# Performance work log

Measured on AMD Instinct MI355X. Metric: run time of the kernel, lower is better.

## Reference

```python
import jax, jax.numpy as jnp
import numpy as np
import math

DIM = 1024
NUM_HEADS = 16
HEAD_DIM = DIM // NUM_HEADS
EPS = 1e-6
DILATED = 2
WINDOW = 2  # window_size init arg; actual window = L * WINDOW per side


def setup_inputs() -> dict:
    key = jax.random.key(0)
    ks = jax.random.split(key, 14)
    B, S = 1, 8704
    x = jax.random.normal(ks[0], (B, S, DIM), jnp.float32)
    ang = jax.random.uniform(ks[1], (S, HEAD_DIM // 2), jnp.float32, -jnp.pi, jnp.pi)
    freqs_cos = jnp.cos(ang)
    freqs_sin = jnp.sin(ang)
    def lin(k):
        return 0.02 * jax.random.normal(k, (DIM, DIM), jnp.float32)
    def bias(k):
        return 0.01 * jax.random.normal(k, (DIM,), jnp.float32)
    return {
        'x': x, 'freqs_cos': freqs_cos, 'freqs_sin': freqs_sin,
        'wq': lin(ks[2]), 'bq': bias(ks[3]),
        'wk': lin(ks[4]), 'bk': bias(ks[5]),
        'wv': lin(ks[6]), 'bv': bias(ks[7]),
        'wo': lin(ks[8]), 'bo': bias(ks[9]),
        'gq': 1.0 + 0.02 * jax.random.normal(ks[10], (DIM,), jnp.float32),
        'gk': 1.0 + 0.02 * jax.random.normal(ks[11], (DIM,), jnp.float32),
        'f': 34, 'L': 256,
    }


def rmsnorm(h, g):
    return h * jax.lax.rsqrt(jnp.mean(h * h, axis=-1, keepdims=True) + EPS) * g


def rope(h, cos, sin):
    # h: [B,S,D] viewed as interleaved complex pairs per head, rotated by unit freqs
    B, S, D = h.shape
    hp = h.reshape(B, S, NUM_HEADS, HEAD_DIM // 2, 2)
    a, b = hp[..., 0], hp[..., 1]
    c = cos[None, :, None, :]
    s = sin[None, :, None, :]
    ra = a * c - b * s
    rb = a * s + b * c
    return jnp.stack([ra, rb], axis=-1).reshape(B, S, D)


def windowed_attention(q, k, v, w):
    # sliding-window attention: query i attends keys j with |i-j| <= w (inclusive)
    B, S, D = q.shape
    H, hd = NUM_HEADS, HEAD_DIM
    def heads(t):
        return t.reshape(B, S, H, hd).transpose(0, 2, 1, 3)  # [B,H,S,hd]
    qh, kh, vh = heads(q), heads(k), heads(v)
    C = w  # block size == window -> only 3 neighbor key blocks per query block
    pad = (-S) % C
    Sp = S + pad
    nb = Sp // C
    def blocks(t):
        return jnp.pad(t, ((0, 0), (0, 0), (0, pad), (0, 0))).reshape(B, H, nb, C, hd)
    qb = blocks(qh)
    def win(t):
        tb = jnp.pad(blocks(t), ((0, 0), (0, 0), (1, 1), (0, 0), (0, 0)))
        return jnp.concatenate([tb[:, :, i:i + nb] for i in range(3)], axis=3)  # [B,H,nb,3C,hd]
    kw_, vw_ = win(kh), win(vh)
    scores = jnp.einsum('bhnqd,bhnkd->bhnqk', qb, kw_) * (1.0 / math.sqrt(hd))
    qi = jnp.arange(nb)[:, None, None] * C + jnp.arange(C)[None, :, None]      # [nb,C,1]
    kj = (jnp.arange(nb)[:, None, None] - 1) * C + jnp.arange(3 * C)[None, None, :]  # [nb,1,3C]
    valid = (kj >= 0) & (kj < S) & (qi - kj <= w) & (kj - qi <= w)
    scores = jnp.where(valid, scores, -1e9)
    p = jax.nn.softmax(scores, axis=-1)
    o = jnp.einsum('bhnqk,bhnkd->bhnqd', p, vw_)
    return o.reshape(B, H, Sp, hd)[:, :, :S].transpose(0, 2, 1, 3).reshape(B, S, D)


def reference(x, freqs_cos, freqs_sin, wq, bq, wk, bk, wv, bv, wo, bo, gq, gk, f, L):
    B, S, D = x.shape
    q = rope(rmsnorm(x @ wq + bq, gq), freqs_cos, freqs_sin)
    k = rope(rmsnorm(x @ wk + bk, gk), freqs_cos, freqs_sin)
    v = x @ wv + bv
    w = L * WINDOW
    use_dilated = DILATED > 1 and S // (DILATED * L) > 1
    if use_dilated:
        blk = DILATED * L
        pad_len = blk - S % blk  # == blk when S % blk == 0 (faithful to torch code)
        Sp = S + pad_len
        n = Sp // blk
        def padd(t):
            return jnp.pad(t, ((0, 0), (0, pad_len), (0, 0)))
        def dil(t):
            # 'b (n d l) c -> (b d) (n l) c'
            return t.reshape(B, n, DILATED, L, D).transpose(0, 2, 1, 3, 4).reshape(B * DILATED, n * L, D)
        q, k, v = dil(padd(q)), dil(padd(k)), dil(padd(v))
    o = windowed_attention(q, k, v, w)
    out = o @ wo + bo
    if use_dilated:
        # '(b d) (n l) c -> b (n d l) c', then drop pad
        out = out.reshape(B, DILATED, n, L, D).transpose(0, 2, 1, 3, 4).reshape(B, n * DILATED * L, D)
        out = out[:, :S]
    return out
```

## Files before the change

kernel.cpp:

```cpp
#include <hip/hip_runtime.h>
#include <hip/hip_bf16.h>
#include <stdint.h>

#define DIM 1024
#define NH 16
#define HD 64
#define S_ORIG 8704
#define WIN 512

typedef __attribute__((ext_vector_type(8))) short short8;
typedef __attribute__((ext_vector_type(4))) float f32x4;

__device__ __forceinline__ float bf2f(unsigned short u) {
    return __uint_as_float(((unsigned int)u) << 16);
}
__device__ __forceinline__ unsigned short f2bf(float f) {
    unsigned int x = __float_as_uint(f);
    unsigned int r = x + 0x7fffu + ((x >> 16) & 1u);
    return (unsigned short)(r >> 16);
}
__device__ __forceinline__ unsigned int cvtpk(float lo, float hi) {
    unsigned int r;
    asm("v_cvt_pk_bf16_f32 %0, %1, %2" : "=v"(r) : "v"(lo), "v"(hi));
    return r;
}
__device__ __forceinline__ float fexp2(float x) {
#if __has_builtin(__builtin_amdgcn_exp2f)
    return __builtin_amdgcn_exp2f(x);
#else
    float r;
    asm("v_exp_f32 %0, %1" : "=v"(r) : "v"(x));
    return r;
#endif
}

#define GLD_LDS(gptr, lptr) \
    __builtin_amdgcn_global_load_lds((const __attribute__((address_space(1))) void*)(gptr), \
                                     (__attribute__((address_space(3))) void*)(lptr), 16, 0, 0)

#define FBAR() do { __asm__ volatile("" ::: "memory"); \
                    __builtin_amdgcn_s_barrier(); \
                    __asm__ volatile("" ::: "memory"); } while (0)

__global__ __launch_bounds__(256) void prep(const float* __restrict__ x,
                                            unsigned short* __restrict__ xb,
                                            const float* __restrict__ w0,
                                            const float* __restrict__ w1,
                                            const float* __restrict__ w2,
                                            const float* __restrict__ w3,
                                            unsigned short* __restrict__ wt) {
    __shared__ float ts[64][65];
    const int bx = blockIdx.x;
    const int t = threadIdx.x;
    if (bx < 8704) {
        int i = (bx * 256 + t) * 4;
        float4 v = *(const float4*)(x + i);
        ushort4 o;
        o.x = f2bf(v.x); o.y = f2bf(v.y); o.z = f2bf(v.z); o.w = f2bf(v.w);
        *(ushort4*)(xb + i) = o;
        return;
    }
    const int b = bx - 8704;
    const int z = b >> 8;
    const int rem = b & 255;
    const int kb = (rem >> 4) * 64, nb = (rem & 15) * 64;
    const float* w = z == 0 ? w0 : z == 1 ? w1 : z == 2 ? w2 : w3;
    unsigned short* o = wt + (size_t)z * DIM * DIM;
    const int c = t & 63, r4 = t >> 6;
#pragma unroll
    for (int rr = 0; rr < 16; rr++) {
        int row = rr * 4 + r4;
        ts[row][c] = w[(size_t)(kb + row) * DIM + nb + c];
    }
    __syncthreads();
#pragma unroll
    for (int rr = 0; rr < 16; rr++) {
        int nl = rr * 4 + r4;
        o[(size_t)(nb + nl) * DIM + kb + c] = f2bf(ts[c][nl]);
    }
}

__device__ __forceinline__ void gemm_step(const unsigned short* __restrict__ pa,
                                          const unsigned short* __restrict__ pb,
                                          int wr, int wc, int r, int jsw,
                                          f32x4 acc[4][4]) {
    short8 af[4], bfr[4];
#pragma unroll
    for (int i = 0; i < 4; i++)
        af[i] = *(const short8*)&pa[(wr * 64 + i * 16 + r) * 32 + jsw];
#pragma unroll
    for (int j = 0; j < 4; j++)
        bfr[j] = *(const short8*)&pb[(wc * 64 + j * 16 + r) * 32 + jsw];
#pragma unroll
    for (int i = 0; i < 4; i++)
#pragma unroll
        for (int j = 0; j < 4; j++)
            acc[i][j] = __builtin_amdgcn_mfma_f32_16x16x32_bf16(af[i], bfr[j], acc[i][j], 0, 0, 0);
}

template <int OUTF32>
__global__ __launch_bounds__(256) void gemm_bf16(const unsigned short* __restrict__ A,
                                                 const unsigned short* __restrict__ Bt,
                                                 const float* __restrict__ b0,
                                                 const float* __restrict__ b1,
                                                 const float* __restrict__ b2,
                                                 void* __restrict__ Cout) {
    __shared__ __align__(16) unsigned short As[3][128 * 32];
    __shared__ __align__(16) unsigned short Bs[3][128 * 32];
    const int z = blockIdx.z;
    const unsigned short* B = Bt + (size_t)z * DIM * DIM;
    const float* bias = z == 0 ? b0 : (z == 1 ? b1 : b2);
    const int m0 = blockIdx.x * 128, n0 = blockIdx.y * 128;
    const int tid = threadIdx.x;
    const int lane = tid & 63, wv = tid >> 6;
    const int wr = wv >> 1, wc = wv & 1;
    const int quad = lane >> 4, r = lane & 15;

    f32x4 acc[4][4];
#pragma unroll
    for (int i = 0; i < 4; i++)
#pragma unroll
        for (int j = 0; j < 4; j++)
#pragma unroll
            for (int t4 = 0; t4 < 4; t4++) acc[i][j][t4] = 0.0f;

    const unsigned short* a_base = A + (size_t)m0 * DIM;
    const unsigned short* b_base = B + (size_t)n0 * DIM;
    const int c0 = wv * 128 + lane;
    const int r0 = c0 >> 2, o0 = (((c0 & 3) ^ ((c0 >> 3) & 3))) * 8;
    const int c1 = c0 + 64;
    const int r1 = c1 >> 2, o1 = (((c1 & 3) ^ ((c1 >> 3) & 3))) * 8;
    const int ld0 = (wv * 128) * 8, ld1 = (wv * 128 + 64) * 8;

    const int jsw = (quad ^ ((r >> 1) & 3)) * 8;

#define ISSUE_STEP(k0_, abuf_, bbuf_) do {                                  \
        GLD_LDS(a_base + (size_t)r0 * DIM + (k0_) + o0, (abuf_) + ld0);     \
        GLD_LDS(a_base + (size_t)r1 * DIM + (k0_) + o1, (abuf_) + ld1);     \
        GLD_LDS(b_base + (size_t)r0 * DIM + (k0_) + o0, (bbuf_) + ld0);     \
        GLD_LDS(b_base + (size_t)r1 * DIM + (k0_) + o1, (bbuf_) + ld1);     \
    } while (0)

    unsigned short *pa0 = &As[0][0], *pa1 = &As[1][0], *pa2 = &As[2][0];
    unsigned short *pb0 = &Bs[0][0], *pb1 = &Bs[1][0], *pb2 = &Bs[2][0];

    ISSUE_STEP(0, pa0, pb0);
    ISSUE_STEP(32, pa1, pb1);

#pragma unroll 3
    for (int k0 = 0; k0 < DIM - 64; k0 += 32) {
        FBAR();
        ISSUE_STEP(k0 + 64, pa2, pb2);
        __asm__ volatile("s_waitcnt vmcnt(8)" ::: "memory");
        __builtin_amdgcn_sched_barrier(0);
        FBAR();
        gemm_step(pa0, pb0, wr, wc, r, jsw, acc);
        unsigned short* t;
        t = pa0; pa0 = pa1; pa1 = pa2; pa2 = t;
        t = pb0; pb0 = pb1; pb1 = pb2; pb2 = t;
    }
    __asm__ volatile("s_waitcnt vmcnt(4)" ::: "memory");
    __builtin_amdgcn_sched_barrier(0);
    FBAR();
    gemm_step(pa0, pb0, wr, wc, r, jsw, acc);
    {
        unsigned short* t;
        t = pa0; pa0 = pa1; pa1 = pa2; pa2 = t;
        t = pb0; pb0 = pb1; pb1 = pb2; pb2 = t;
    }
    __asm__ volatile("s_waitcnt vmcnt(0)" ::: "memory");
    __builtin_amdgcn_sched_barrier(0);
    FBAR();
    gemm_step(pa0, pb0, wr, wc, r, jsw, acc);
#undef ISSUE_STEP

#pragma unroll
    for (int i = 0; i < 4; i++) {
        const int row = m0 + wr * 64 + i * 16 + quad * 4;
#pragma unroll
        for (int j = 0; j < 4; j++) {
            const int col = n0 + wc * 64 + j * 16 + r;
            const float bvl = bias[col];
#pragma unroll
            for (int t4 = 0; t4 < 4; t4++) {
                float vv = acc[i][j][t4] + bvl;
                if (OUTF32) {
                    ((float*)Cout)[(size_t)(row + t4) * DIM + col] = vv;
                } else {
                    ((unsigned short*)Cout)[(size_t)z * S_ORIG * DIM + (size_t)(row + t4) * DIM + col] = f2bf(vv);
                }
            }
        }
    }
}

__global__ __launch_bounds__(256) void norm_rope(unsigned short* __restrict__ hq,
                                                 unsigned short* __restrict__ hk,
                                                 const float* __restrict__ gq,
                                                 const float* __restrict__ gk,
                                                 const float* __restrict__ fcos,
                                                 const float* __restrict__ fsin) {
    const int z = blockIdx.y;
    unsigned short* h = z == 0 ? hq : hk;
    const float* g = z == 0 ? gq : gk;
    const int w = threadIdx.x >> 6, lane = threadIdx.x & 63;
    const int srow = blockIdx.x * 4 + w;
    unsigned short* hp = h + (size_t)srow * DIM;
    const int p0 = lane * 8, p1 = 512 + lane * 8;

    union { int4 i4; unsigned short u[8]; } r0, r1, o0, o1;
    r0.i4 = *(const int4*)(hp + p0);
    r1.i4 = *(const int4*)(hp + p1);
    float v[16];
#pragma unroll
    for (int j = 0; j < 8; j++) { v[j] = bf2f(r0.u[j]); v[8 + j] = bf2f(r1.u[j]); }

    float ss = 0.0f;
#pragma unroll
    for (int j = 0; j < 16; j++) ss += v[j] * v[j];
#pragma unroll
    for (int off = 1; off < 64; off <<= 1) ss += __shfl_xor(ss, off, 64);
    const float rinv = rsqrtf(ss * (1.0f / DIM) + 1e-6f);

    float4 ga = *(const float4*)(g + p0), gb = *(const float4*)(g + p0 + 4);
    float4 gc = *(const float4*)(g + p1), gd = *(const float4*)(g + p1 + 4);
    const float* gg[4] = {&ga.x, &gb.x, &gc.x, &gd.x};
#pragma unroll
    for (int q4 = 0; q4 < 4; q4++)
#pragma unroll
        for (int j = 0; j < 4; j++) v[q4 * 4 + j] *= rinv * gg[q4][j];

    const int i0 = (p0 & 63) >> 1;
    float4 cs = *(const float4*)(fcos + (size_t)srow * 32 + i0);
    float4 sn = *(const float4*)(fsin + (size_t)srow * 32 + i0);
    const float* cp = &cs.x;
    const float* sp = &sn.x;
#pragma unroll
    for (int seg = 0; seg < 2; seg++) {
        unsigned short* uo = seg == 0 ? o0.u : o1.u;
#pragma unroll
        for (int pr = 0; pr < 4; pr++) {
            const float a = v[seg * 8 + pr * 2], b = v[seg * 8 + pr * 2 + 1];
            uo[pr * 2]     = f2bf(a * cp[pr] - b * sp[pr]);
            uo[pr * 2 + 1] = f2bf(a * sp[pr] + b * cp[pr]);
        }
    }
    *(int4*)(hp + p0) = o0.i4;
    *(int4*)(hp + p1) = o1.i4;
}

__device__ __forceinline__ void qstep(const unsigned short* __restrict__ Ks,
                                      const unsigned short* __restrict__ Vt,
                                      unsigned short* __restrict__ pw,
                                      int jsw0, int jsw1, int quad, int r16,
                                      int kbase, int qi, bool edge,
                                      const short8* __restrict__ qf,
                                      f32x4* __restrict__ oacc, float& lsum) {
    f32x4 sv[4];
#pragma unroll
    for (int nt = 0; nt < 4; nt++) {
        const int row = (nt * 16 + r16) * 64;
        short8 k0f = *(const short8*)&Ks[row + jsw0];
        short8 k1f = *(const short8*)&Ks[row + jsw1];
        f32x4 a = {0.0f, 0.0f, 0.0f, 0.0f};
        a = __builtin_amdgcn_mfma_f32_16x16x32_bf16(k0f, qf[0], a, 0, 0, 0);
        a = __builtin_amdgcn_mfma_f32_16x16x32_bf16(k1f, qf[1], a, 0, 0, 0);
        sv[nt] = a;
    }
#pragma unroll
    for (int nt = 0; nt < 4; nt++) {
        float p[4];
#pragma unroll
        for (int rr = 0; rr < 4; rr++) {
            float e = fexp2(sv[nt][rr]);
            if (edge) {
                const int kj = kbase + nt * 16 + quad * 4 + rr;
                const int dl = qi - kj;
                if (dl > WIN || dl < -WIN) e = 0.0f;
            }
            p[rr] = e;
        }
        lsum += (p[0] + p[1]) + (p[2] + p[3]);
        uint2 pk;
        pk.x = cvtpk(p[0], p[1]);
        pk.y = cvtpk(p[2], p[3]);
        *(uint2*)&pw[r16 * 72 + nt * 16 + quad * 4] = pk;
    }
    __asm__ volatile("s_waitcnt lgkmcnt(0)" ::: "memory");
    short8 pf0 = *(const short8*)&pw[r16 * 72 + quad * 8];
    short8 pf1 = *(const short8*)&pw[r16 * 72 + 32 + quad * 8];
#pragma unroll
    for (int nt = 0; nt < 4; nt++) {
        short8 v0f = *(const short8*)&Vt[(nt * 16 + r16) * 72 + quad * 8];
        short8 v1f = *(const short8*)&Vt[(nt * 16 + r16) * 72 + 32 + quad * 8];
        oacc[nt] = __builtin_amdgcn_mfma_f32_16x16x32_bf16(v0f, pf0, oacc[nt], 0, 0, 0);
        oacc[nt] = __builtin_amdgcn_mfma_f32_16x16x32_bf16(v1f, pf1, oacc[nt], 0, 0, 0);
    }
}

__device__ __forceinline__ void pack_write_v(unsigned short* __restrict__ Vt,
                                             int4 a0i, int4 a1i, int vt_d0, int vt_kk) {
    union { int4 i4; unsigned int w[4]; } a0, a1;
    a0.i4 = a0i; a1.i4 = a1i;
#pragma unroll
    for (int dw = 0; dw < 4; dw++) {
        unsigned int lo = __builtin_amdgcn_perm(a1.w[dw], a0.w[dw], 0x05040100u);
        unsigned int hi = __builtin_amdgcn_perm(a1.w[dw], a0.w[dw], 0x07060302u);
        *(unsigned int*)&Vt[(vt_d0 + dw * 2) * 72 + vt_kk] = lo;
        *(unsigned int*)&Vt[(vt_d0 + dw * 2 + 1) * 72 + vt_kk] = hi;
    }
}

__global__ __launch_bounds__(256) void attn(const unsigned short* __restrict__ qkv,
                                            unsigned short* __restrict__ ob) {
    __shared__ __align__(16) unsigned short Ks[2][64 * 64];
    __shared__ __align__(16) unsigned short Vt[64 * 72];
    __shared__ __align__(16) unsigned short Ps[4][16 * 72];

    const int head = blockIdx.x >> 1;
    const int d = blockIdx.x & 1;
    const int t0 = blockIdx.y * 2, t1 = t0 + 1;
    const int tid = threadIdx.x;
    const int lane = tid & 63, wv = tid >> 6;
    const int quad = lane >> 4, r16 = lane & 15;

    const unsigned short* qb = qkv;
    const unsigned short* kb = qkv + (size_t)S_ORIG * DIM;
    const unsigned short* vb = qkv + (size_t)2 * S_ORIG * DIM;

    const int qi0 = t0 * 64 + wv * 16 + r16;
    const int qi1 = qi0 + 64;
    const int og_q0 = ((qi0 >> 8) << 9) + d * 256 + (qi0 & 255);
    const int og_q1 = ((qi1 >> 8) << 9) + d * 256 + (qi1 & 255);
    short8 qf0[2], qf1[2];
    {
        const float QSC = 0.125f * 1.44269504088896f;
        const unsigned short* qr0 = qb + (size_t)og_q0 * DIM + head * HD + quad * 8;
        const unsigned short* qr1 = qb + (size_t)og_q1 * DIM + head * HD + quad * 8;
#pragma unroll
        for (int c = 0; c < 2; c++) {
            union { int4 i4; unsigned short u[8]; short8 s8; } i0v, i1v, a0v, a1v;
            i0v.i4 = *(const int4*)(qr0 + c * 32);
            i1v.i4 = *(const int4*)(qr1 + c * 32);
#pragma unroll
            for (int j = 0; j < 8; j++) {
                a0v.u[j] = f2bf(bf2f(i0v.u[j]) * QSC);
                a1v.u[j] = f2bf(bf2f(i1v.u[j]) * QSC);
            }
            qf0[c] = a0v.s8;
            qf1[c] = a1v.s8;
        }
    }

    f32x4 oacc0[4], oacc1[4];
    float lsum0 = 0.0f, lsum1 = 0.0f;
#pragma unroll
    for (int nt = 0; nt < 4; nt++)
#pragma unroll
        for (int rr = 0; rr < 4; rr++) { oacc0[nt][rr] = 0.0f; oacc1[nt][rr] = 0.0f; }

    const int kt_lo = (t0 - 8 > 0) ? (t0 - 8) : 0;
    const int kt_hi = (t1 + 8 < 67) ? (t1 + 8) : 67;

    const int krow0 = tid >> 3;
    const int kgc = ((tid & 7) ^ (krow0 & 7)) * 8;

    const int vt_kk = (tid & 31) * 2, vt_d0 = (tid >> 5) * 8;

    const int jsw0 = (quad ^ (r16 & 7)) * 8;
    const int jsw1 = jsw0 ^ 32;

    unsigned short* pw = &Ps[wv][0];

#define ISSUE_K(kbase_, bufb_) do {                                              \
        const int kj0_ = (kbase_) + krow0;                                       \
        const int ok0_ = ((kj0_ >> 8) << 9) + d * 256 + (kj0_ & 255);            \
        GLD_LDS(kb + (size_t)ok0_ * DIM + head * HD + kgc, (bufb_) + wv * 512);  \
        const int kj1_ = kj0_ + 32;                                              \
        const int ok1_ = ((kj1_ >> 8) << 9) + d * 256 + (kj1_ & 255);            \
        GLD_LDS(kb + (size_t)ok1_ * DIM + head * HD + kgc, (bufb_) + 2048 + wv * 512); \
    } while (0)

#define LOAD_V(kbase_, a0_, a1_) do {                                            \
        const int kj_ = (kbase_) + vt_kk;                                        \
        const int ok_ = ((kj_ >> 8) << 9) + d * 256 + (kj_ & 255);               \
        (a0_) = *(const int4*)(vb + (size_t)ok_ * DIM + head * HD + vt_d0);      \
        (a1_) = *(const int4*)(vb + (size_t)(ok_ + 1) * DIM + head * HD + vt_d0);\
    } while (0)

    ISSUE_K(kt_lo * 64, &Ks[0][0]);
    int4 vc0, vc1;
    LOAD_V(kt_lo * 64, vc0, vc1);

    int cur = 0;
    for (int kt = kt_lo; kt <= kt_hi; kt++) {
        const int kbase = kt * 64;
        FBAR();

        const int knb = ((kt < kt_hi) ? (kt + 1) : kt_hi) * 64;
        ISSUE_K(knb, &Ks[cur ^ 1][0]);
        int4 vn0, vn1;
        LOAD_V(knb, vn0, vn1);

        __asm__ volatile("s_waitcnt vmcnt(4)" ::: "memory");
        __builtin_amdgcn_sched_barrier(0);

        pack_write_v(&Vt[0], vc0, vc1, vt_d0, vt_kk);
        __asm__ volatile("s_waitcnt lgkmcnt(0)" ::: "memory");
        FBAR();

        if (kt <= t0 + 8)
            qstep(&Ks[cur][0], Vt, pw, jsw0, jsw1, quad, r16, kbase, qi0,
                  (kt == t0 - 8) || (kt == t0 + 8), qf0, oacc0, lsum0);
        if (kt >= t1 - 8)
            qstep(&Ks[cur][0], Vt, pw, jsw0, jsw1, quad, r16, kbase, qi1,
                  (kt == t1 - 8) || (kt == t1 + 8), qf1, oacc1, lsum1);

        vc0 = vn0; vc1 = vn1;
        cur ^= 1;
    }
#undef ISSUE_K
#undef LOAD_V

    __asm__ volatile("" :: "v"(vc0.x), "v"(vc0.y), "v"(vc0.z), "v"(vc0.w),
                          "v"(vc1.x), "v"(vc1.y), "v"(vc1.z), "v"(vc1.w));
    __asm__ volatile("s_waitcnt vmcnt(0)" ::: "memory");

    lsum0 += __shfl_xor(lsum0, 16, 64);
    lsum0 += __shfl_xor(lsum0, 32, 64);
    lsum1 += __shfl_xor(lsum1, 16, 64);
    lsum1 += __shfl_xor(lsum1, 32, 64);
    {
        const int cnt0 = (qi0 + WIN < 4607 ? qi0 + WIN : 4607) - 4351;
        if (cnt0 > 0) lsum0 += (float)cnt0;
        const int cnt1 = (qi1 + WIN < 4607 ? qi1 + WIN : 4607) - 4351;
        if (cnt1 > 0) lsum1 += (float)cnt1;
    }
    const float linv0 = 1.0f / lsum0;
    const float linv1 = 1.0f / lsum1;

#pragma unroll
    for (int nt = 0; nt < 4; nt++) {
        ushort4 o0, o1;
        o0.x = f2bf(oacc0[nt][0] * linv0);
        o0.y = f2bf(oacc0[nt][1] * linv0);
        o0.z = f2bf(oacc0[nt][2] * linv0);
        o0.w = f2bf(oacc0[nt][3] * linv0);
        *(ushort4*)&ob[(size_t)og_q0 * DIM + head * HD + nt * 16 + quad * 4] = o0;
        o1.x = f2bf(oacc1[nt][0] * linv1);
        o1.y = f2bf(oacc1[nt][1] * linv1);
        o1.z = f2bf(oacc1[nt][2] * linv1);
        o1.w = f2bf(oacc1[nt][3] * linv1);
        *(ushort4*)&ob[(size_t)og_q1 * DIM + head * HD + nt * 16 + quad * 4] = o1;
    }
}

extern "C" void kernel_launch(void* const* d_in, const int* in_sizes, int n_in,
                              void* d_out, int out_size, void* d_ws, size_t ws_size,
                              hipStream_t stream) {
    const float* x    = (const float*)d_in[0];
    const float* fcos = (const float*)d_in[1];
    const float* fsin = (const float*)d_in[2];
    const float* wq   = (const float*)d_in[3];
    const float* bq   = (const float*)d_in[4];
    const float* wk   = (const float*)d_in[5];
    const float* bk   = (const float*)d_in[6];
    const float* wv   = (const float*)d_in[7];
    const float* bv   = (const float*)d_in[8];
    const float* wo   = (const float*)d_in[9];
    const float* bo   = (const float*)d_in[10];
    const float* gq   = (const float*)d_in[11];
    const float* gk   = (const float*)d_in[12];

    char* ws = (char*)d_ws;
    unsigned short* xb = (unsigned short*)(ws);
    unsigned short* wt = (unsigned short*)(ws + 17825792);
    unsigned short* h  = (unsigned short*)(ws + 26214400);
    unsigned short* ob = (unsigned short*)(ws + 79691776);
    float* outp = (float*)d_out;

    prep<<<9728, 256, 0, stream>>>(x, xb, wq, wk, wv, wo, wt);
    gemm_bf16<0><<<dim3(68, 8, 3), 256, 0, stream>>>(xb, wt, bq, bk, bv, (void*)h);
    norm_rope<<<dim3(2176, 2), 256, 0, stream>>>(h, h + (size_t)S_ORIG * DIM, gq, gk, fcos, fsin);
    attn<<<dim3(32, 34), 256, 0, stream>>>(h, ob);
    gemm_bf16<1><<<dim3(68, 8, 1), 256, 0, stream>>>(ob, wt + (size_t)3 * DIM * DIM, bo, bo, bo, (void*)outp);
}
```

Before: 302.6 us.

## Switch attention to 32x32x16 MFMA with register-resident P via permlane32 swap

New measurement: 305.4 us. Within noise of the previous version (+0.9%).

```diff
diff --git a/kernel.cpp b/kernel.cpp
--- a/kernel.cpp
+++ b/kernel.cpp
@@ -10,6 +10,7 @@
 
 typedef __attribute__((ext_vector_type(8))) short short8;
 typedef __attribute__((ext_vector_type(4))) float f32x4;
+typedef __attribute__((ext_vector_type(16))) float f32x16;
 
 __device__ __forceinline__ float bf2f(unsigned short u) {
     return __uint_as_float(((unsigned int)u) << 16);
@@ -249,115 +250,85 @@
     *(int4*)(hp + p1) = o1.i4;
 }
 
-__device__ __forceinline__ void qstep(const unsigned short* __restrict__ Ks,
-                                      const unsigned short* __restrict__ Vt,
-                                      unsigned short* __restrict__ pw,
-                                      int jsw0, int jsw1, int quad, int r16,
-                                      int kbase, int qi, bool edge,
-                                      const short8* __restrict__ qf,
-                                      f32x4* __restrict__ oacc, float& lsum) {
-    f32x4 sv[4];
-#pragma unroll
-    for (int nt = 0; nt < 4; nt++) {
-        const int row = (nt * 16 + r16) * 64;
-        short8 k0f = *(const short8*)&Ks[row + jsw0];
-        short8 k1f = *(const short8*)&Ks[row + jsw1];
-        f32x4 a = {0.0f, 0.0f, 0.0f, 0.0f};
-        a = __builtin_amdgcn_mfma_f32_16x16x32_bf16(k0f, qf[0], a, 0, 0, 0);
-        a = __builtin_amdgcn_mfma_f32_16x16x32_bf16(k1f, qf[1], a, 0, 0, 0);
-        sv[nt] = a;
-    }
-#pragma unroll
-    for (int nt = 0; nt < 4; nt++) {
-        float p[4];
-#pragma unroll
-        for (int rr = 0; rr < 4; rr++) {
-            float e = fexp2(sv[nt][rr]);
-            if (edge) {
-                const int kj = kbase + nt * 16 + quad * 4 + rr;
-                const int dl = qi - kj;
-                if (dl > WIN || dl < -WIN) e = 0.0f;
-            }
-            p[rr] = e;
+__device__ __forceinline__ void softmax16(f32x16& s, int kk0, int hi4, int qi,
+                                          bool edge, float& lsum) {
+#pragma unroll
+    for (int reg = 0; reg < 16; reg++) {
+        float e = fexp2(s[reg]);
+        if (edge) {
+            const int kj = kk0 + (reg & 3) + 8 * (reg >> 2) + hi4;
+            const int dl = qi - kj;
+            if (dl > WIN || dl < -WIN) e = 0.0f;
         }
-        lsum += (p[0] + p[1]) + (p[2] + p[3]);
-        uint2 pk;
-        pk.x = cvtpk(p[0], p[1]);
-        pk.y = cvtpk(p[2], p[3]);
-        *(uint2*)&pw[r16 * 72 + nt * 16 + quad * 4] = pk;
-    }
-    __asm__ volatile("s_waitcnt lgkmcnt(0)" ::: "memory");
-    short8 pf0 = *(const short8*)&pw[r16 * 72 + quad * 8];
-    short8 pf1 = *(const short8*)&pw[r16 * 72 + 32 + quad * 8];
-#pragma unroll
-    for (int nt = 0; nt < 4; nt++) {
-        short8 v0f = *(const short8*)&Vt[(nt * 16 + r16) * 72 + quad * 8];
-        short8 v1f = *(const short8*)&Vt[(nt * 16 + r16) * 72 + 32 + quad * 8];
-        oacc[nt] = __builtin_amdgcn_mfma_f32_16x16x32_bf16(v0f, pf0, oacc[nt], 0, 0, 0);
-        oacc[nt] = __builtin_amdgcn_mfma_f32_16x16x32_bf16(v1f, pf1, oacc[nt], 0, 0, 0);
-    }
+        s[reg] = e;
+        lsum += e;
+    }
+}
+
+__device__ __forceinline__ short8 mkfrag(const f32x16& p, int base) {
+    unsigned int a0 = cvtpk(p[base + 0], p[base + 1]);
+    unsigned int b0 = cvtpk(p[base + 4], p[base + 5]);
+    unsigned int a1 = cvtpk(p[base + 2], p[base + 3]);
+    unsigned int b1 = cvtpk(p[base + 6], p[base + 7]);
+    asm volatile("v_permlane32_swap_b32 %0, %1" : "+v"(a0), "+v"(b0));
+    asm volatile("v_permlane32_swap_b32 %0, %1" : "+v"(a1), "+v"(b1));
+    union { unsigned int w[4]; short8 s; } u;
+    u.w[0] = a0; u.w[1] = a1; u.w[2] = b0; u.w[3] = b1;
+    return u.s;
 }
 
 __device__ __forceinline__ void pack_write_v(unsigned short* __restrict__ Vt,
-                                             int4 a0i, int4 a1i, int vt_d0, int vt_kk) {
+                                             int4 a0i, int4 a1i, int vt_d0, int vkc, int vko) {
     union { int4 i4; unsigned int w[4]; } a0, a1;
     a0.i4 = a0i; a1.i4 = a1i;
 #pragma unroll
     for (int dw = 0; dw < 4; dw++) {
         unsigned int lo = __builtin_amdgcn_perm(a1.w[dw], a0.w[dw], 0x05040100u);
-        unsigned int hi = __builtin_amdgcn_perm(a1.w[dw], a0.w[dw], 0x07060302u);
-        *(unsigned int*)&Vt[(vt_d0 + dw * 2) * 72 + vt_kk] = lo;
-        *(unsigned int*)&Vt[(vt_d0 + dw * 2 + 1) * 72 + vt_kk] = hi;
+        unsigned int hw = __builtin_amdgcn_perm(a1.w[dw], a0.w[dw], 0x07060302u);
+        *(unsigned int*)&Vt[(vt_d0 + dw * 2) * 64 + ((vkc ^ (dw * 2)) << 3) + vko] = lo;
+        *(unsigned int*)&Vt[(vt_d0 + dw * 2 + 1) * 64 + ((vkc ^ (dw * 2 + 1)) << 3) + vko] = hw;
     }
 }
 
 __global__ __launch_bounds__(256) void attn(const unsigned short* __restrict__ qkv,
                                             unsigned short* __restrict__ ob) {
     __shared__ __align__(16) unsigned short Ks[2][64 * 64];
-    __shared__ __align__(16) unsigned short Vt[64 * 72];
-    __shared__ __align__(16) unsigned short Ps[4][16 * 72];
+    __shared__ __align__(16) unsigned short Vt[64 * 64];
 
     const int head = blockIdx.x >> 1;
     const int d = blockIdx.x & 1;
     const int t0 = blockIdx.y * 2, t1 = t0 + 1;
     const int tid = threadIdx.x;
     const int lane = tid & 63, wv = tid >> 6;
-    const int quad = lane >> 4, r16 = lane & 15;
+    const int hi = lane >> 5, q32 = lane & 31;
+    const int sw8 = (q32 & 7);
 
     const unsigned short* qb = qkv;
     const unsigned short* kb = qkv + (size_t)S_ORIG * DIM;
     const unsigned short* vb = qkv + (size_t)2 * S_ORIG * DIM;
 
-    const int qi0 = t0 * 64 + wv * 16 + r16;
-    const int qi1 = qi0 + 64;
-    const int og_q0 = ((qi0 >> 8) << 9) + d * 256 + (qi0 & 255);
-    const int og_q1 = ((qi1 >> 8) << 9) + d * 256 + (qi1 & 255);
-    short8 qf0[2], qf1[2];
+    const int tw = t0 + (wv >> 1);
+    const int qi = tw * 64 + (wv & 1) * 32 + q32;
+    const int og_q = ((qi >> 8) << 9) + d * 256 + (qi & 255);
+
+    short8 qf[4];
     {
         const float QSC = 0.125f * 1.44269504088896f;
-        const unsigned short* qr0 = qb + (size_t)og_q0 * DIM + head * HD + quad * 8;
-        const unsigned short* qr1 = qb + (size_t)og_q1 * DIM + head * HD + quad * 8;
-#pragma unroll
-        for (int c = 0; c < 2; c++) {
-            union { int4 i4; unsigned short u[8]; short8 s8; } i0v, i1v, a0v, a1v;
-            i0v.i4 = *(const int4*)(qr0 + c * 32);
-            i1v.i4 = *(const int4*)(qr1 + c * 32);
-#pragma unroll
-            for (int j = 0; j < 8; j++) {
-                a0v.u[j] = f2bf(bf2f(i0v.u[j]) * QSC);
-                a1v.u[j] = f2bf(bf2f(i1v.u[j]) * QSC);
-            }
-            qf0[c] = a0v.s8;
-            qf1[c] = a1v.s8;
+        const unsigned short* qrow = qb + (size_t)og_q * DIM + head * HD + hi * 8;
+#pragma unroll
+        for (int kd = 0; kd < 4; kd++) {
+            union { int4 i4; unsigned short u[8]; short8 s8; } iv, ov;
+            iv.i4 = *(const int4*)(qrow + kd * 16);
+#pragma unroll
+            for (int j = 0; j < 8; j++) ov.u[j] = f2bf(bf2f(iv.u[j]) * QSC);
+            qf[kd] = ov.s8;
         }
     }
 
-    f32x4 oacc0[4], oacc1[4];
-    float lsum0 = 0.0f, lsum1 = 0.0f;
-#pragma unroll
-    for (int nt = 0; nt < 4; nt++)
-#pragma unroll
-        for (int rr = 0; rr < 4; rr++) { oacc0[nt][rr] = 0.0f; oacc1[nt][rr] = 0.0f; }
+    f32x16 o0, o1;
+#pragma unroll
+    for (int i = 0; i < 16; i++) { o0[i] = 0.0f; o1[i] = 0.0f; }
+    float lsum = 0.0f;
 
     const int kt_lo = (t0 - 8 > 0) ? (t0 - 8) : 0;
     const int kt_hi = (t1 + 8 < 67) ? (t1 + 8) : 67;
@@ -366,11 +337,7 @@
     const int kgc = ((tid & 7) ^ (krow0 & 7)) * 8;
 
     const int vt_kk = (tid & 31) * 2, vt_d0 = (tid >> 5) * 8;
-
-    const int jsw0 = (quad ^ (r16 & 7)) * 8;
-    const int jsw1 = jsw0 ^ 32;
-
-    unsigned short* pw = &Ps[wv][0];
+    const int vkc = vt_kk >> 3, vko = vt_kk & 7;
 
 #define ISSUE_K(kbase_, bufb_) do {                                              \
         const int kj0_ = (kbase_) + krow0;                                       \
@@ -405,16 +372,42 @@
         __asm__ volatile("s_waitcnt vmcnt(4)" ::: "memory");
         __builtin_amdgcn_sched_barrier(0);
 
-        pack_write_v(&Vt[0], vc0, vc1, vt_d0, vt_kk);
+        pack_write_v(&Vt[0], vc0, vc1, vt_d0, vkc, vko);
         __asm__ volatile("s_waitcnt lgkmcnt(0)" ::: "memory");
         FBAR();
 
-        if (kt <= t0 + 8)
-            qstep(&Ks[cur][0], Vt, pw, jsw0, jsw1, quad, r16, kbase, qi0,
-                  (kt == t0 - 8) || (kt == t0 + 8), qf0, oacc0, lsum0);
-        if (kt >= t1 - 8)
-            qstep(&Ks[cur][0], Vt, pw, jsw0, jsw1, quad, r16, kbase, qi1,
-                  (kt == t1 - 8) || (kt == t1 + 8), qf1, oacc1, lsum1);
+        if (kt >= tw - 8 && kt <= tw + 8) {
+            const bool edge = (kt == tw - 8) || (kt == tw + 8);
+            const unsigned short* K = &Ks[cur][0];
+
+            f32x16 s0, s1;
+#pragma unroll
+            for (int i = 0; i < 16; i++) { s0[i] = 0.0f; s1[i] = 0.0f; }
+#pragma unroll
+            for (int kd = 0; kd < 4; kd++) {
+                const int c = ((kd * 2 + hi) ^ sw8) << 3;
+                short8 k0 = *(const short8*)&K[q32 * 64 + c];
+                short8 k1 = *(const short8*)&K[(32 + q32) * 64 + c];
+                s0 = __builtin_amdgcn_mfma_f32_32x32x16_bf16(k0, qf[kd], s0, 0, 0, 0);
+                s1 = __builtin_amdgcn_mfma_f32_32x32x16_bf16(k1, qf[kd], s1, 0, 0, 0);
+            }
+
+            const int hi4 = hi * 4;
+            softmax16(s0, kbase, hi4, qi, edge, lsum);
+            softmax16(s1, kbase + 32, hi4, qi, edge, lsum);
+            short8 pf0 = mkfrag(s0, 0), pf1 = mkfrag(s0, 8);
+            short8 pf2 = mkfrag(s1, 0), pf3 = mkfrag(s1, 8);
+
+#pragma unroll
+            for (int kw = 0; kw < 4; kw++) {
+                const int c = ((kw * 2 + hi) ^ sw8) << 3;
+                short8 v0 = *(const short8*)&Vt[q32 * 64 + c];
+                short8 v1 = *(const short8*)&Vt[(32 + q32) * 64 + c];
+                const short8 pf = kw == 0 ? pf0 : kw == 1 ? pf1 : kw == 2 ? pf2 : pf3;
+                o0 = __builtin_amdgcn_mfma_f32_32x32x16_bf16(v0, pf, o0, 0, 0, 0);
+                o1 = __builtin_amdgcn_mfma_f32_32x32x16_bf16(v1, pf, o1, 0, 0, 0);
+            }
+        }
 
         vc0 = vn0; vc1 = vn1;
         cur ^= 1;
@@ -426,32 +419,27 @@
                           "v"(vc1.x), "v"(vc1.y), "v"(vc1.z), "v"(vc1.w));
     __asm__ volatile("s_waitcnt vmcnt(0)" ::: "memory");
 
-    lsum0 += __shfl_xor(lsum0, 16, 64);
-    lsum0 += __shfl_xor(lsum0, 32, 64);
-    lsum1 += __shfl_xor(lsum1, 16, 64);
-    lsum1 += __shfl_xor(lsum1, 32, 64);
+    lsum += __shfl_xor(lsum, 32, 64);
     {
-        const int cnt0 = (qi0 + WIN < 4607 ? qi0 + WIN : 4607) - 4351;
-        if (cnt0 > 0) lsum0 += (float)cnt0;
-        const int cnt1 = (qi1 + WIN < 4607 ? qi1 + WIN : 4607) - 4351;
-        if (cnt1 > 0) lsum1 += (float)cnt1;
-    }
-    const float linv0 = 1.0f / lsum0;
-    const float linv1 = 1.0f / lsum1;
-
-#pragma unroll
-    for (int nt = 0; nt < 4; nt++) {
-        ushort4 o0, o1;
-        o0.x = f2bf(oacc0[nt][0] * linv0);
-        o0.y = f2bf(oacc0[nt][1] * linv0);
-        o0.z = f2bf(oacc0[nt][2] * linv0);
-        o0.w = f2bf(oacc0[nt][3] * linv0);
-        *(ushort4*)&ob[(size_t)og_q0 * DIM + head * HD + nt * 16 + quad * 4] = o0;
-        o1.x = f2bf(oacc1[nt][0] * linv1);
-        o1.y = f2bf(oacc1[nt][1] * linv1);
-        o1.z = f2bf(oacc1[nt][2] * linv1);
-        o1.w = f2bf(oacc1[nt][3] * linv1);
-        *(ushort4*)&ob[(size_t)og_q1 * DIM + head * HD + nt * 16 + quad * 4] = o1;
+        const int cnt = (qi + WIN < 4607 ? qi + WIN : 4607) - 4351;
+        if (cnt > 0) lsum += (float)cnt;
+    }
+    const float linv = 1.0f / lsum;
+
+    unsigned short* obase = ob + (size_t)og_q * DIM + head * HD + hi * 4;
+#pragma unroll
+    for (int g = 0; g < 4; g++) {
+        ushort4 u0, u1;
+        u0.x = f2bf(o0[g * 4 + 0] * linv);
+        u0.y = f2bf(o0[g * 4 + 1] * linv);
+        u0.z = f2bf(o0[g * 4 + 2] * linv);
+        u0.w = f2bf(o0[g * 4 + 3] * linv);
+        *(ushort4*)(obase + g * 8) = u0;
+        u1.x = f2bf(o1[g * 4 + 0] * linv);
+        u1.y = f2bf(o1[g * 4 + 1] * linv);
+        u1.z = f2bf(o1[g * 4 + 2] * linv);
+        u1.w = f2bf(o1[g * 4 + 3] * linv);
+        *(ushort4*)(obase + 32 + g * 8) = u1;
     }
 }
 
```
